# Kernel optimization log

Measured on AMD Instinct MI355X. Metric: run time of the kernel, lower is better.

Reference implementation:

```python
import jax, jax.numpy as jnp
import numpy as np

H = 16
D_MODEL = 1024
D_K = D_MODEL // H


def setup_inputs() -> dict:
    key = jax.random.key(0)
    ks = jax.random.split(key, 10)
    B, S = 2, 2048
    q = jax.random.normal(ks[0], (B, S, D_MODEL), dtype=jnp.float32)
    k = jax.random.normal(ks[1], (B, S, D_MODEL), dtype=jnp.float32)
    v = jax.random.normal(ks[2], (B, S, D_MODEL), dtype=jnp.float32)
    mask = jax.random.randint(ks[3], (B, 1, S), 0, 2, dtype=jnp.int32)
    s = 1.0 / np.sqrt(D_MODEL)
    w_q = jax.random.normal(ks[4], (D_MODEL, D_MODEL), dtype=jnp.float32) * s
    b_q = jnp.zeros((D_MODEL,), dtype=jnp.float32)
    w_v = jax.random.normal(ks[5], (D_MODEL, D_MODEL), dtype=jnp.float32) * s
    b_v = jnp.zeros((D_MODEL,), dtype=jnp.float32)
    w_o = jax.random.normal(ks[6], (D_MODEL, D_MODEL), dtype=jnp.float32) * s
    b_o = jnp.zeros((D_MODEL,), dtype=jnp.float32)
    return {"q": q, "k": k, "v": v, "mask": mask,
            "w_q": w_q, "b_q": b_q, "w_v": w_v, "b_v": b_v,
            "w_o": w_o, "b_o": b_o}


def _split_heads(x, B):
    # [B, S, D] -> [B, H, S, d_k]
    return x.reshape(B, -1, H, D_K).transpose(0, 2, 1, 3)


def reference(q, k, v, mask, w_q, b_q, w_v, b_v, w_o, b_o):
    B = q.shape[0]
    # NOTE: source uses w_q for BOTH q and k (w_k is dead code) — reproduced faithfully.
    qh = _split_heads(q @ w_q.T + b_q, B)
    kh = _split_heads(k @ w_q.T + b_q, B)
    vh = _split_heads(v @ w_v.T + b_v, B)
    scores = jnp.einsum('bhqd,bhkd->bhqk', qh, kh) * (1.0 / np.sqrt(D_K))
    # mask [B,1,S] -> unsqueeze(1) -> [B,1,1,S], broadcast over heads and query dim
    m = mask[:, None, :, :]
    scores = jnp.where(m == 0, -jnp.inf, scores)
    attn = jax.nn.softmax(scores, axis=-1)  # dropout is identity (eval / p=0)
    out = jnp.einsum('bhqk,bhkd->bhqd', attn, vh)
    out = out.transpose(0, 2, 1, 3).reshape(B, -1, D_MODEL)
    out = out @ w_o.T + b_o
    return out, attn
```

## Files before the change

kernel.cpp:

```cpp
#include <hip/hip_runtime.h>

#define S_LEN 2048
#define DMODEL 1024
#define NH 16
#define DK 64
#define BATCH 2
#define BS (BATCH * S_LEN)

typedef _Float16 f16;
typedef _Float16 f16x8 __attribute__((ext_vector_type(8)));
typedef _Float16 f16x4 __attribute__((ext_vector_type(4)));
typedef float f32x4 __attribute__((ext_vector_type(4)));

__device__ __forceinline__ f32x4 mfma16(f16x8 a, f16x8 b, f32x4 c) {
  return __builtin_amdgcn_mfma_f32_16x16x32_f16(a, b, c, 0, 0, 0);
}

template <typename AT, int MODE>
__device__ __forceinline__ void gemm_body(const AT* __restrict__ A,
                                          const float* __restrict__ W,
                                          const float* __restrict__ bias,
                                          void* __restrict__ outp, float scale,
                                          f16 (*As)[40], f16 (*Ws)[40]) {
  const int t = threadIdx.x;
  const int m0 = blockIdx.y * 128;
  const int n0 = blockIdx.x * 128;
  const int wave = t >> 6, lane = t & 63;
  const int wr = wave >> 1, wc = wave & 1;
  const int lcol = lane & 15, kq = lane >> 4;

  f32x4 acc[4][4];
  const f32x4 zero = {0.f, 0.f, 0.f, 0.f};
#pragma unroll
  for (int i = 0; i < 4; ++i)
#pragma unroll
    for (int j = 0; j < 4; ++j) acc[i][j] = zero;

  for (int k0 = 0; k0 < DMODEL; k0 += 32) {
    if constexpr (sizeof(AT) == 4) {
#pragma unroll
      for (int i = 0; i < 4; ++i) {
        int f = t + i * 256;
        int r = f >> 3, c = (f & 7) << 2;
        const float4 v = *reinterpret_cast<const float4*>(
            &((const float*)A)[(size_t)(m0 + r) * DMODEL + k0 + c]);
        f16x4 h = {(f16)v.x, (f16)v.y, (f16)v.z, (f16)v.w};
        *reinterpret_cast<f16x4*>(&As[r][c]) = h;
      }
    } else {
#pragma unroll
      for (int i = 0; i < 2; ++i) {
        int f = t + i * 256;
        int r = f >> 2, c = (f & 3) << 3;
        *reinterpret_cast<f16x8*>(&As[r][c]) = *reinterpret_cast<const f16x8*>(
            &((const f16*)A)[(size_t)(m0 + r) * DMODEL + k0 + c]);
      }
    }
#pragma unroll
    for (int i = 0; i < 4; ++i) {
      int f = t + i * 256;
      int r = f >> 3, c = (f & 7) << 2;
      const float4 v = *reinterpret_cast<const float4*>(
          &W[(size_t)(n0 + r) * DMODEL + k0 + c]);
      f16x4 h = {(f16)v.x, (f16)v.y, (f16)v.z, (f16)v.w};
      *reinterpret_cast<f16x4*>(&Ws[r][c]) = h;
    }
    __syncthreads();
    f16x8 af[4], bf[4];
#pragma unroll
    for (int fr = 0; fr < 4; ++fr)
      af[fr] = *reinterpret_cast<const f16x8*>(&As[wr * 64 + fr * 16 + lcol][kq * 8]);
#pragma unroll
    for (int fc = 0; fc < 4; ++fc)
      bf[fc] = *reinterpret_cast<const f16x8*>(&Ws[wc * 64 + fc * 16 + lcol][kq * 8]);
#pragma unroll
    for (int fr = 0; fr < 4; ++fr)
#pragma unroll
      for (int fc = 0; fc < 4; ++fc) acc[fr][fc] = mfma16(af[fr], bf[fc], acc[fr][fc]);
    __syncthreads();
  }

#pragma unroll
  for (int fc = 0; fc < 4; ++fc) {
    const int gj = n0 + wc * 64 + fc * 16 + lcol;
    const float bv = bias[gj];
#pragma unroll
    for (int fr = 0; fr < 4; ++fr) {
#pragma unroll
      for (int r = 0; r < 4; ++r) {
        const int gi = m0 + wr * 64 + fr * 16 + kq * 4 + r;
        const float val = (acc[fr][fc][r] + bv) * scale;
        if constexpr (MODE == 0) {
          const int b = gi >> 11, s = gi & 2047, h = gj >> 6, dk = gj & 63;
          ((f16*)outp)[(((size_t)(b * NH + h) * S_LEN) + s) * DK + dk] = (f16)val;
        } else if constexpr (MODE == 1) {
          const int b = gi >> 11, s = gi & 2047, h = gj >> 6, dk = gj & 63;
          ((f16*)outp)[(((size_t)(b * NH + h) * DK) + dk) * S_LEN + s] = (f16)val;
        } else {
          ((float*)outp)[(size_t)gi * DMODEL + gj] = val;
        }
      }
    }
  }
}

__global__ __launch_bounds__(256, 2) void qkv_gemm(
    const float* __restrict__ q, const float* __restrict__ k,
    const float* __restrict__ v, const float* __restrict__ w_q,
    const float* __restrict__ b_q, const float* __restrict__ w_v,
    const float* __restrict__ b_v, f16* __restrict__ qh, f16* __restrict__ kh,
    f16* __restrict__ vhT) {
  __shared__ f16 As[128][40];
  __shared__ f16 Ws[128][40];
  if (blockIdx.z == 0)
    gemm_body<float, 0>(q, w_q, b_q, qh, 0.125f, As, Ws);
  else if (blockIdx.z == 1)
    gemm_body<float, 0>(k, w_q, b_q, kh, 1.0f, As, Ws);
  else
    gemm_body<float, 1>(v, w_v, b_v, vhT, 1.0f, As, Ws);
}

__global__ __launch_bounds__(256, 2) void gemm_out(const f16* __restrict__ A,
                                                   const float* __restrict__ W,
                                                   const float* __restrict__ bias,
                                                   float* __restrict__ outp) {
  __shared__ f16 As[128][40];
  __shared__ f16 Ws[128][40];
  gemm_body<f16, 2>(A, W, bias, outp, 1.0f, As, Ws);
}

__global__ __launch_bounds__(256, 2) void stats_kernel(
    const f16* __restrict__ qh, const f16* __restrict__ kh,
    const int* __restrict__ mask, float* __restrict__ l_out) {
  __shared__ f16 Ks[64][72];
  __shared__ int msk[S_LEN];
  const int t = threadIdx.x;
  const int bh = blockIdx.y, b = bh >> 4;
  const int i0 = blockIdx.x * 128;
  const int wave = t >> 6, lane = t & 63;
  const int lcol = lane & 15, kq = lane >> 4;
  const int rbase = i0 + wave * 32;
  const f16* Q = qh + (size_t)bh * S_LEN * DK;
  const f16* K = kh + (size_t)bh * S_LEN * DK;

  for (int i = t; i < S_LEN; i += 256) msk[i] = mask[b * S_LEN + i];

  f16x8 aq[2][2];
#pragma unroll
  for (int rt = 0; rt < 2; ++rt)
#pragma unroll
    for (int ks = 0; ks < 2; ++ks)
      aq[rt][ks] = *reinterpret_cast<const f16x8*>(
          &Q[(size_t)(rbase + rt * 16 + lcol) * DK + ks * 32 + kq * 8]);

  float l_acc[2][4];
#pragma unroll
  for (int rt = 0; rt < 2; ++rt)
#pragma unroll
    for (int r = 0; r < 4; ++r) l_acc[rt][r] = 0.f;

  for (int j0 = 0; j0 < S_LEN; j0 += 64) {
    __syncthreads();
#pragma unroll
    for (int i = 0; i < 2; ++i) {
      int f = t + i * 256;
      int r = f >> 3, c = (f & 7) << 3;
      *reinterpret_cast<f16x8*>(&Ks[r][c]) =
          *reinterpret_cast<const f16x8*>(&K[(size_t)(j0 + r) * DK + c]);
    }
    __syncthreads();
#pragma unroll
    for (int jt = 0; jt < 4; ++jt) {
      const f16x8 bk0 = *reinterpret_cast<const f16x8*>(&Ks[jt * 16 + lcol][kq * 8]);
      const f16x8 bk1 =
          *reinterpret_cast<const f16x8*>(&Ks[jt * 16 + lcol][kq * 8 + 32]);
      const int mv = msk[j0 + jt * 16 + lcol];
#pragma unroll
      for (int rt = 0; rt < 2; ++rt) {
        f32x4 c = {0.f, 0.f, 0.f, 0.f};
        c = mfma16(aq[rt][0], bk0, c);
        c = mfma16(aq[rt][1], bk1, c);
#pragma unroll
        for (int r = 0; r < 4; ++r)
          l_acc[rt][r] += mv ? __expf(c[r]) : 0.f;
      }
    }
  }
#pragma unroll
  for (int rt = 0; rt < 2; ++rt)
#pragma unroll
    for (int r = 0; r < 4; ++r) {
      float es = l_acc[rt][r];
#pragma unroll
      for (int o = 1; o < 16; o <<= 1) es += __shfl_xor(es, o);
      if (lcol == 0) {
        const int row = (bh << 11) + rbase + rt * 16 + kq * 4 + r;
        l_out[row] = es;
      }
    }
}

__global__ __launch_bounds__(256, 2) void attn_pv_kernel(
    const f16* __restrict__ qh, const f16* __restrict__ kh,
    const f16* __restrict__ vhT, const int* __restrict__ mask,
    const float* __restrict__ l_in, float* __restrict__ attn,
    f16* __restrict__ ctx) {
  __shared__ f16 Ks[64][72];
  __shared__ f16 Vs[64][72];
  __shared__ f16 Ps[4][32][72];
  __shared__ int msk[S_LEN];
  const int t = threadIdx.x;
  const int bh = blockIdx.y, b = bh >> 4, h = bh & 15;
  const int i0 = blockIdx.x * 128;
  const int wave = t >> 6, lane = t & 63;
  const int lcol = lane & 15, kq = lane >> 4;
  const int rbase = i0 + wave * 32;
  const f16* Q = qh + (size_t)bh * S_LEN * DK;
  const f16* K = kh + (size_t)bh * S_LEN * DK;
  const f16* V = vhT + (size_t)bh * DK * S_LEN;
  float* Sc = attn + (size_t)bh * S_LEN * S_LEN;

  for (int i = t; i < S_LEN; i += 256) msk[i] = mask[b * S_LEN + i];

  f16x8 aq[2][2];
#pragma unroll
  for (int rt = 0; rt < 2; ++rt)
#pragma unroll
    for (int ks = 0; ks < 2; ++ks)
      aq[rt][ks] = *reinterpret_cast<const f16x8*>(
          &Q[(size_t)(rbase + rt * 16 + lcol) * DK + ks * 32 + kq * 8]);

  float il[2][4];
#pragma unroll
  for (int rt = 0; rt < 2; ++rt)
#pragma unroll
    for (int r = 0; r < 4; ++r) {
      const int row = (bh << 11) + rbase + rt * 16 + kq * 4 + r;
      il[rt][r] = 1.0f / l_in[row];
    }

  f32x4 o[2][4];
  const f32x4 zero = {0.f, 0.f, 0.f, 0.f};
#pragma unroll
  for (int rt = 0; rt < 2; ++rt)
#pragma unroll
    for (int d = 0; d < 4; ++d) o[rt][d] = zero;

  for (int j0 = 0; j0 < S_LEN; j0 += 64) {
    __syncthreads();
#pragma unroll
    for (int i = 0; i < 2; ++i) {
      int f = t + i * 256;
      int r = f >> 3, c = (f & 7) << 3;
      *reinterpret_cast<f16x8*>(&Ks[r][c]) =
          *reinterpret_cast<const f16x8*>(&K[(size_t)(j0 + r) * DK + c]);
      *reinterpret_cast<f16x8*>(&Vs[r][c]) =
          *reinterpret_cast<const f16x8*>(&V[(size_t)r * S_LEN + j0 + c]);
    }
    __syncthreads();
#pragma unroll
    for (int jt = 0; jt < 4; ++jt) {
      const f16x8 bk0 = *reinterpret_cast<const f16x8*>(&Ks[jt * 16 + lcol][kq * 8]);
      const f16x8 bk1 =
          *reinterpret_cast<const f16x8*>(&Ks[jt * 16 + lcol][kq * 8 + 32]);
      const int mv = msk[j0 + jt * 16 + lcol];
#pragma unroll
      for (int rt = 0; rt < 2; ++rt) {
        f32x4 c = {0.f, 0.f, 0.f, 0.f};
        c = mfma16(aq[rt][0], bk0, c);
        c = mfma16(aq[rt][1], bk1, c);
#pragma unroll
        for (int r = 0; r < 4; ++r) {
          const float p = mv ? __expf(c[r]) * il[rt][r] : 0.f;
          Sc[((size_t)(rbase + rt * 16 + kq * 4 + r) << 11) + j0 + jt * 16 + lcol] =
              p;
          Ps[wave][rt * 16 + kq * 4 + r][jt * 16 + lcol] = (f16)p;
        }
      }
    }
#pragma unroll
    for (int ks = 0; ks < 2; ++ks) {
      f16x8 ap[2], bv[4];
#pragma unroll
      for (int rt = 0; rt < 2; ++rt)
        ap[rt] =
            *reinterpret_cast<const f16x8*>(&Ps[wave][rt * 16 + lcol][ks * 32 + kq * 8]);
#pragma unroll
      for (int d = 0; d < 4; ++d)
        bv[d] = *reinterpret_cast<const f16x8*>(&Vs[d * 16 + lcol][ks * 32 + kq * 8]);
#pragma unroll
      for (int rt = 0; rt < 2; ++rt)
#pragma unroll
        for (int d = 0; d < 4; ++d) o[rt][d] = mfma16(ap[rt], bv[d], o[rt][d]);
    }
  }

#pragma unroll
  for (int d = 0; d < 4; ++d) {
    const int dk = d * 16 + lcol;
#pragma unroll
    for (int rt = 0; rt < 2; ++rt)
#pragma unroll
      for (int r = 0; r < 4; ++r) {
        const int s = rbase + rt * 16 + kq * 4 + r;
        ctx[(size_t)(b * S_LEN + s) * DMODEL + h * DK + dk] = (f16)o[rt][d][r];
      }
  }
}

extern "C" void kernel_launch(void* const* d_in, const int* in_sizes, int n_in,
                              void* d_out, int out_size, void* d_ws, size_t ws_size,
                              hipStream_t stream) {
  const float* q = (const float*)d_in[0];
  const float* k = (const float*)d_in[1];
  const float* v = (const float*)d_in[2];
  const int* mask = (const int*)d_in[3];
  const float* w_q = (const float*)d_in[4];
  const float* b_q = (const float*)d_in[5];
  const float* w_v = (const float*)d_in[6];
  const float* b_v = (const float*)d_in[7];
  const float* w_o = (const float*)d_in[8];
  const float* b_o = (const float*)d_in[9];

  float* out = (float*)d_out;
  float* attn = out + (size_t)BS * DMODEL;

  f16* qh = (f16*)d_ws;
  f16* kh = qh + (size_t)BS * DMODEL;
  f16* vhT = kh + (size_t)BS * DMODEL;
  f16* ctx = vhT + (size_t)BS * DMODEL;
  float* l_arr = (float*)(ctx + (size_t)BS * DMODEL);

  qkv_gemm<<<dim3(8, 32, 3), 256, 0, stream>>>(q, k, v, w_q, b_q, w_v, b_v, qh,
                                               kh, vhT);
  stats_kernel<<<dim3(16, 32), 256, 0, stream>>>(qh, kh, mask, l_arr);
  attn_pv_kernel<<<dim3(16, 32), 256, 0, stream>>>(qh, kh, vhT, mask, l_arr,
                                                   attn, ctx);
  gemm_out<<<dim3(8, 32), 256, 0, stream>>>(ctx, w_o, b_o, out);
}
```

Measured before the change: 871.2 us.

## Stage attention probabilities through LDS for coalesced stores; read K/V directly

The probability tile is now staged in shared memory as fp32, and each wave writes it to the attention output in coalesced float4 rows instead of scattered per-element stores. The same staged values are converted to fp16 for the PV MFMA. K and V tiles are no longer staged in LDS: each lane loads its operand fragments straight from global memory, which removes both per-iteration block barriers in the stats and attention kernels. This trades LDS reuse across waves for cache-dependent global reads and per-element fp16 conversion work. The fp32 Ps reads (row stride 66) may also hit bank conflicts.

Result: no change. 877.3 us (+0.7%).

```diff
diff --git a/kernel.cpp b/kernel.cpp
--- a/kernel.cpp
+++ b/kernel.cpp
@@ -132,7 +132,6 @@
 __global__ __launch_bounds__(256, 2) void stats_kernel(
     const f16* __restrict__ qh, const f16* __restrict__ kh,
     const int* __restrict__ mask, float* __restrict__ l_out) {
-  __shared__ f16 Ks[64][72];
   __shared__ int msk[S_LEN];
   const int t = threadIdx.x;
   const int bh = blockIdx.y, b = bh >> 4;
@@ -159,21 +158,14 @@
 #pragma unroll
     for (int r = 0; r < 4; ++r) l_acc[rt][r] = 0.f;
 
+  __syncthreads();
+
   for (int j0 = 0; j0 < S_LEN; j0 += 64) {
-    __syncthreads();
-#pragma unroll
-    for (int i = 0; i < 2; ++i) {
-      int f = t + i * 256;
-      int r = f >> 3, c = (f & 7) << 3;
-      *reinterpret_cast<f16x8*>(&Ks[r][c]) =
-          *reinterpret_cast<const f16x8*>(&K[(size_t)(j0 + r) * DK + c]);
-    }
-    __syncthreads();
 #pragma unroll
     for (int jt = 0; jt < 4; ++jt) {
-      const f16x8 bk0 = *reinterpret_cast<const f16x8*>(&Ks[jt * 16 + lcol][kq * 8]);
-      const f16x8 bk1 =
-          *reinterpret_cast<const f16x8*>(&Ks[jt * 16 + lcol][kq * 8 + 32]);
+      const f16* Krow = &K[(size_t)(j0 + jt * 16 + lcol) * DK + kq * 8];
+      const f16x8 bk0 = *reinterpret_cast<const f16x8*>(Krow);
+      const f16x8 bk1 = *reinterpret_cast<const f16x8*>(Krow + 32);
       const int mv = msk[j0 + jt * 16 + lcol];
 #pragma unroll
       for (int rt = 0; rt < 2; ++rt) {
@@ -181,8 +173,7 @@
         c = mfma16(aq[rt][0], bk0, c);
         c = mfma16(aq[rt][1], bk1, c);
 #pragma unroll
-        for (int r = 0; r < 4; ++r)
-          l_acc[rt][r] += mv ? __expf(c[r]) : 0.f;
+        for (int r = 0; r < 4; ++r) l_acc[rt][r] += mv ? __expf(c[r]) : 0.f;
       }
     }
   }
@@ -200,14 +191,13 @@
     }
 }
 
+#define PST 66
 __global__ __launch_bounds__(256, 2) void attn_pv_kernel(
     const f16* __restrict__ qh, const f16* __restrict__ kh,
     const f16* __restrict__ vhT, const int* __restrict__ mask,
     const float* __restrict__ l_in, float* __restrict__ attn,
     f16* __restrict__ ctx) {
-  __shared__ f16 Ks[64][72];
-  __shared__ f16 Vs[64][72];
-  __shared__ f16 Ps[4][32][72];
+  __shared__ float Ps[4][32][PST];
   __shared__ int msk[S_LEN];
   const int t = threadIdx.x;
   const int bh = blockIdx.y, b = bh >> 4, h = bh & 15;
@@ -246,23 +236,14 @@
 #pragma unroll
     for (int d = 0; d < 4; ++d) o[rt][d] = zero;
 
+  __syncthreads();
+
   for (int j0 = 0; j0 < S_LEN; j0 += 64) {
-    __syncthreads();
-#pragma unroll
-    for (int i = 0; i < 2; ++i) {
-      int f = t + i * 256;
-      int r = f >> 3, c = (f & 7) << 3;
-      *reinterpret_cast<f16x8*>(&Ks[r][c]) =
-          *reinterpret_cast<const f16x8*>(&K[(size_t)(j0 + r) * DK + c]);
-      *reinterpret_cast<f16x8*>(&Vs[r][c]) =
-          *reinterpret_cast<const f16x8*>(&V[(size_t)r * S_LEN + j0 + c]);
-    }
-    __syncthreads();
 #pragma unroll
     for (int jt = 0; jt < 4; ++jt) {
-      const f16x8 bk0 = *reinterpret_cast<const f16x8*>(&Ks[jt * 16 + lcol][kq * 8]);
-      const f16x8 bk1 =
-          *reinterpret_cast<const f16x8*>(&Ks[jt * 16 + lcol][kq * 8 + 32]);
+      const f16* Krow = &K[(size_t)(j0 + jt * 16 + lcol) * DK + kq * 8];
+      const f16x8 bk0 = *reinterpret_cast<const f16x8*>(Krow);
+      const f16x8 bk1 = *reinterpret_cast<const f16x8*>(Krow + 32);
       const int mv = msk[j0 + jt * 16 + lcol];
 #pragma unroll
       for (int rt = 0; rt < 2; ++rt) {
@@ -272,22 +253,32 @@
 #pragma unroll
         for (int r = 0; r < 4; ++r) {
           const float p = mv ? __expf(c[r]) * il[rt][r] : 0.f;
-          Sc[((size_t)(rbase + rt * 16 + kq * 4 + r) << 11) + j0 + jt * 16 + lcol] =
-              p;
-          Ps[wave][rt * 16 + kq * 4 + r][jt * 16 + lcol] = (f16)p;
+          Ps[wave][rt * 16 + kq * 4 + r][jt * 16 + lcol] = p;
         }
       }
+    }
+#pragma unroll
+    for (int ps = 0; ps < 8; ++ps) {
+      const int lr = ps * 4 + kq;
+      const float4 vv = *reinterpret_cast<const float4*>(&Ps[wave][lr][lcol * 4]);
+      *reinterpret_cast<float4*>(
+          &Sc[((size_t)(rbase + lr) << 11) + j0 + lcol * 4]) = vv;
     }
 #pragma unroll
     for (int ks = 0; ks < 2; ++ks) {
       f16x8 ap[2], bv[4];
 #pragma unroll
-      for (int rt = 0; rt < 2; ++rt)
-        ap[rt] =
-            *reinterpret_cast<const f16x8*>(&Ps[wave][rt * 16 + lcol][ks * 32 + kq * 8]);
+      for (int rt = 0; rt < 2; ++rt) {
+        const float* pr = &Ps[wave][rt * 16 + lcol][ks * 32 + kq * 8];
+        f16x8 a;
+#pragma unroll
+        for (int e = 0; e < 8; ++e) a[e] = (f16)pr[e];
+        ap[rt] = a;
+      }
 #pragma unroll
       for (int d = 0; d < 4; ++d)
-        bv[d] = *reinterpret_cast<const f16x8*>(&Vs[d * 16 + lcol][ks * 32 + kq * 8]);
+        bv[d] = *reinterpret_cast<const f16x8*>(
+            &V[(size_t)(d * 16 + lcol) * S_LEN + j0 + ks * 32 + kq * 8]);
 #pragma unroll
       for (int rt = 0; rt < 2; ++rt)
 #pragma unroll
```
